# Kernel tuning notes

Hardware: AMD Instinct MI355X
Metric: run time of the kernel (lower is better)

The kernel has to match this reference:

```python
import jax, jax.numpy as jnp
import numpy as np

H = 64
VOCAB = 64
SLOTS = 8
EPS = 1e-5


def _layernorm(x, gamma, beta):
    mu = jnp.mean(x, axis=-1, keepdims=True)
    var = jnp.mean(jnp.square(x - mu), axis=-1, keepdims=True)
    return (x - mu) * jax.lax.rsqrt(var + EPS) * gamma + beta


def setup_inputs() -> dict:
    key = jax.random.key(0)
    ks = jax.random.split(key, 20)
    B, L = 1024, 2048
    s = 0.05
    inp = {
        "seq": jax.random.randint(ks[0], (B, L), 0, VOCAB, dtype=jnp.int64),
        "embed": jax.random.normal(ks[1], (VOCAB, H), jnp.float32) * s,
        "w1": jax.random.normal(ks[2], (2 * H, H), jnp.float32) * s,
        "b1": jnp.zeros((2 * H,), jnp.float32),
        "w2": jax.random.normal(ks[3], (H, 2 * H), jnp.float32) * s,
        "b2": jnp.zeros((H,), jnp.float32),
        "gamma": jnp.ones((H,), jnp.float32),
        "beta": jnp.zeros((H,), jnp.float32),
        "gate_w": jax.random.normal(ks[4], (1, H), jnp.float32) * s,
        "gate_b": jnp.zeros((1,), jnp.float32),
        "qi_w": jax.random.normal(ks[5], (H, H), jnp.float32) * s,
        "qi_b": jnp.zeros((H,), jnp.float32),
        "sk_w": jax.random.normal(ks[6], (H, H), jnp.float32) * s,
        "sk_b": jnp.zeros((H,), jnp.float32),
        "qr_w": jax.random.normal(ks[7], (H, H), jnp.float32) * s,
        "qr_b": jnp.zeros((H,), jnp.float32),
        "out_w": jax.random.normal(ks[8], (VOCAB, H), jnp.float32) * s,
        "out_b": jnp.zeros((VOCAB,), jnp.float32),
    }
    return inp


def reference(seq, embed, w1, b1, w2, b2, gamma, beta, gate_w, gate_b,
              qi_w, qi_b, sk_w, sk_b, qr_w, qr_b, out_w, out_b):
    # Encoder: embed -> FF residual -> LayerNorm
    h0 = embed[seq]                                  # [B, L, H]
    ff = jax.nn.relu(h0 @ w1.T + b1) @ w2.T + b2     # [B, L, H]
    h = _layernorm(h0 + ff, gamma, beta)             # [B, L, H]

    # Top-k gate over sequence -> gather memory slots
    scores = jnp.squeeze(h @ gate_w.T, -1) + gate_b[0]   # [B, L]
    _, idx = jax.lax.top_k(scores, SLOTS)                # [B, S]
    memory = jnp.take_along_axis(h, idx[:, :, None], axis=1)  # [B, S, H]

    scale = 1.0 / jnp.sqrt(jnp.float32(H))

    # Stage 1: initial read attention over slot keys
    q_init = h[:, -1, :] @ qi_w.T + qi_b                 # [B, H]
    slot_keys = memory @ sk_w.T + sk_b                   # [B, S, H]
    r_attn = jax.nn.softmax(jnp.einsum('bsh,bh->bs', slot_keys, q_init) * scale, axis=-1)
    read = jnp.einsum('bs,bsh->bh', r_attn, memory)
    q_refined = q_init + (read @ qr_w.T + qr_b)          # [B, H]

    # Stage 2: refined attention directly over memory
    attn = jax.nn.softmax(jnp.einsum('bsh,bh->bs', memory, q_refined) * scale, axis=-1)
    pooled = jnp.einsum('bs,bsh->bh', attn, memory)      # [B, H]
    return pooled @ out_w.T + out_b                      # [B, VOCAB]
```

## Files before the change

### kernel.cpp

```cpp
#include <hip/hip_runtime.h>
#include <hip/hip_bf16.h>

#define HD 64
#define LSEQ 2048
#define NBATCH 1024
#define NSLOTS 8

__global__ __launch_bounds__(128) void build_tables_kernel(
    const float* __restrict__ embed, const float* __restrict__ w1, const float* __restrict__ b1,
    const float* __restrict__ w2, const float* __restrict__ b2,
    const float* __restrict__ gamma, const float* __restrict__ beta,
    const float* __restrict__ gate_w, const float* __restrict__ gate_b,
    const float* __restrict__ qi_w, const float* __restrict__ qi_b,
    const float* __restrict__ sk_w, const float* __restrict__ sk_b,
    float* __restrict__ h_table, float* __restrict__ qi_table, float* __restrict__ sk_table,
    float* __restrict__ score)
{
    const int v = blockIdx.x;
    const int tid = threadIdx.x;

    __shared__ __align__(16) float E[HD];
    __shared__ __align__(16) float T1[2 * HD];
    __shared__ __align__(16) float Hrow[HD];

    if (tid < HD) E[tid] = embed[v * HD + tid];
    __syncthreads();

    {
        const float4* w1r = (const float4*)(w1 + tid * HD);
        const float4* E4  = (const float4*)E;
        float t = b1[tid];
        #pragma unroll
        for (int k = 0; k < HD / 4; ++k) {
            float4 a = w1r[k], e = E4[k];
            t = fmaf(a.x, e.x, t); t = fmaf(a.y, e.y, t);
            t = fmaf(a.z, e.z, t); t = fmaf(a.w, e.w, t);
        }
        T1[tid] = fmaxf(t, 0.0f);
    }
    __syncthreads();

    if (tid < HD) {
        const float4* w2r = (const float4*)(w2 + tid * 2 * HD);
        const float4* T4  = (const float4*)T1;
        float x = E[tid] + b2[tid];
        #pragma unroll
        for (int j = 0; j < 2 * HD / 4; ++j) {
            float4 a = w2r[j], t = T4[j];
            x = fmaf(a.x, t.x, x); x = fmaf(a.y, t.y, x);
            x = fmaf(a.z, t.z, x); x = fmaf(a.w, t.w, x);
        }
        float mu = x;
        #pragma unroll
        for (int off = 1; off < 64; off <<= 1) mu += __shfl_xor(mu, off);
        mu *= (1.0f / 64.0f);
        float d = x - mu;
        float var = d * d;
        #pragma unroll
        for (int off = 1; off < 64; off <<= 1) var += __shfl_xor(var, off);
        var *= (1.0f / 64.0f);
        float h = d * rsqrtf(var + 1e-5f) * gamma[tid] + beta[tid];
        Hrow[tid] = h;
        h_table[v * HD + tid] = h;

        float sc = h * gate_w[tid];
        #pragma unroll
        for (int off = 1; off < 64; off <<= 1) sc += __shfl_xor(sc, off);
        if (tid == 0) score[v] = sc + gate_b[0];
    }
    __syncthreads();

    {
        const int i = tid & 63;
        const float* W  = (tid < HD) ? qi_w : sk_w;
        const float* Bv = (tid < HD) ? qi_b : sk_b;
        const float4* Wr = (const float4*)(W + i * HD);
        const float4* H4 = (const float4*)Hrow;
        float acc = Bv[i];
        #pragma unroll
        for (int k = 0; k < HD / 4; ++k) {
            float4 a = Wr[k], h = H4[k];
            acc = fmaf(a.x, h.x, acc); acc = fmaf(a.y, h.y, acc);
            acc = fmaf(a.z, h.z, acc); acc = fmaf(a.w, h.w, acc);
        }
        float* dst = (tid < HD) ? qi_table : sk_table;
        dst[v * HD + i] = acc;
    }
}

__global__ __launch_bounds__(256) void main_kernel(
    const int* __restrict__ seq,
    const float* __restrict__ h_table, const float* __restrict__ qi_table,
    const float* __restrict__ sk_table,
    const float* __restrict__ qr_w, const float* __restrict__ qr_b,
    const float* __restrict__ out_w, const float* __restrict__ out_b,
    const float* __restrict__ score,
    float* __restrict__ out)
{
    const int b    = blockIdx.x;
    const int tid  = threadIdx.x;
    const int w    = tid >> 6;
    const int lane = tid & 63;

    __shared__ int   hist[4][65];
    __shared__ int   slot_tok[NSLOTS];
    __shared__ float sbuf[64];
    __shared__ int   order_s[64];
    __shared__ int   cntb[64];
    __shared__ int   last_s;
    __shared__ __align__(16) float rbuf[64];

    hist[w][lane] = 0;
    if (tid < 64) sbuf[tid] = score[tid];

    const int4* srow4 = (const int4*)(seq + (size_t)b * LSEQ);
    int4 a0 = srow4[tid];
    int4 a1 = srow4[256 + tid];
    if (tid == 255) last_s = a1.w;
    __syncthreads();

    atomicAdd(&hist[w][a0.x], 1); atomicAdd(&hist[w][a0.y], 1);
    atomicAdd(&hist[w][a0.z], 1); atomicAdd(&hist[w][a0.w], 1);
    atomicAdd(&hist[w][a1.x], 1); atomicAdd(&hist[w][a1.y], 1);
    atomicAdd(&hist[w][a1.z], 1); atomicAdd(&hist[w][a1.w], 1);
    __syncthreads();

    if (tid < 64) {
        int cnt = hist[0][tid] + hist[1][tid] + hist[2][tid] + hist[3][tid];
        float st = sbuf[tid];
        int rank = 0;
        for (int u = 0; u < 64; ++u) {
            float su = sbuf[u];
            if (su > st || (su == st && u < tid)) ++rank;
        }
        order_s[rank] = tid;
        hist[0][tid] = cnt;
    }
    __syncthreads();

    if (tid < 64) cntb[tid] = hist[0][order_s[tid]];
    __syncthreads();

    if (tid < 64) {
        int cum = 0;
        for (int u = 0; u < tid; ++u) cum += cntb[u];
        int cnt = cntb[tid];
        int tok = order_s[tid];
        #pragma unroll
        for (int s = 0; s < NSLOTS; ++s)
            if (s >= cum && s < cum + cnt) slot_tok[s] = tok;
    }
    __syncthreads();

    float qk = 0.0f;
    float mrow[NSLOTS];
    const float scale = 0.125f;

    if (tid < 64) {
        int st_[NSLOTS];
        #pragma unroll
        for (int s = 0; s < NSLOTS; ++s) st_[s] = slot_tok[s];

        qk = qi_table[last_s * HD + lane];

        float skrow[NSLOTS];
        #pragma unroll
        for (int s = 0; s < NSLOTS; ++s) {
            mrow[s]  = h_table[st_[s] * HD + lane];
            skrow[s] = sk_table[st_[s] * HD + lane];
        }

        float p[NSLOTS];
        #pragma unroll
        for (int s = 0; s < NSLOTS; ++s) p[s] = skrow[s] * qk;
        #pragma unroll
        for (int off = 1; off < 64; off <<= 1) {
            #pragma unroll
            for (int s = 0; s < NSLOTS; ++s) p[s] += __shfl_xor(p[s], off);
        }
        #pragma unroll
        for (int s = 0; s < NSLOTS; ++s) p[s] *= scale;
        float mx = p[0];
        #pragma unroll
        for (int s = 1; s < NSLOTS; ++s) mx = fmaxf(mx, p[s]);
        float sum = 0.0f, r[NSLOTS];
        #pragma unroll
        for (int s = 0; s < NSLOTS; ++s) { r[s] = expf(p[s] - mx); sum += r[s]; }
        float inv = 1.0f / sum;
        float readk = 0.0f;
        #pragma unroll
        for (int s = 0; s < NSLOTS; ++s) readk = fmaf(r[s] * inv, mrow[s], readk);
        rbuf[lane] = readk;
    }
    __syncthreads();

    float qref = 0.0f;
    if (tid < 64) {
        qref = qk + qr_b[lane];
        const float4* wr = (const float4*)(qr_w + lane * HD);
        const float4* r4 = (const float4*)rbuf;
        #pragma unroll
        for (int j = 0; j < HD / 4; ++j) {
            float4 a = wr[j], rv = r4[j];
            qref = fmaf(a.x, rv.x, qref); qref = fmaf(a.y, rv.y, qref);
            qref = fmaf(a.z, rv.z, qref); qref = fmaf(a.w, rv.w, qref);
        }

        float p2[NSLOTS];
        #pragma unroll
        for (int s = 0; s < NSLOTS; ++s) p2[s] = mrow[s] * qref;
        #pragma unroll
        for (int off = 1; off < 64; off <<= 1) {
            #pragma unroll
            for (int s = 0; s < NSLOTS; ++s) p2[s] += __shfl_xor(p2[s], off);
        }
        #pragma unroll
        for (int s = 0; s < NSLOTS; ++s) p2[s] *= scale;
        float mx = p2[0];
        #pragma unroll
        for (int s = 1; s < NSLOTS; ++s) mx = fmaxf(mx, p2[s]);
        float sum = 0.0f, a[NSLOTS];
        #pragma unroll
        for (int s = 0; s < NSLOTS; ++s) { a[s] = expf(p2[s] - mx); sum += a[s]; }
        float inv = 1.0f / sum;
        float pooled = 0.0f;
        #pragma unroll
        for (int s = 0; s < NSLOTS; ++s) pooled = fmaf(a[s] * inv, mrow[s], pooled);
        rbuf[lane] = pooled;
    }
    __syncthreads();

    if (tid < 64) {
        float acc = out_b[lane];
        const float4* wr = (const float4*)(out_w + lane * HD);
        const float4* r4 = (const float4*)rbuf;
        #pragma unroll
        for (int k = 0; k < HD / 4; ++k) {
            float4 a = wr[k], rv = r4[k];
            acc = fmaf(a.x, rv.x, acc); acc = fmaf(a.y, rv.y, acc);
            acc = fmaf(a.z, rv.z, acc); acc = fmaf(a.w, rv.w, acc);
        }
        out[(size_t)b * HD + lane] = acc;
    }
}

extern "C" void kernel_launch(void* const* d_in, const int* in_sizes, int n_in,
                              void* d_out, int out_size, void* d_ws, size_t ws_size,
                              hipStream_t stream) {
    const int*   seq    = (const int*)  d_in[0];
    const float* embed  = (const float*)d_in[1];
    const float* w1     = (const float*)d_in[2];
    const float* b1     = (const float*)d_in[3];
    const float* w2     = (const float*)d_in[4];
    const float* b2     = (const float*)d_in[5];
    const float* gamma  = (const float*)d_in[6];
    const float* beta   = (const float*)d_in[7];
    const float* gate_w = (const float*)d_in[8];
    const float* gate_b = (const float*)d_in[9];
    const float* qi_w   = (const float*)d_in[10];
    const float* qi_b   = (const float*)d_in[11];
    const float* sk_w   = (const float*)d_in[12];
    const float* sk_b   = (const float*)d_in[13];
    const float* qr_w   = (const float*)d_in[14];
    const float* qr_b   = (const float*)d_in[15];
    const float* out_w  = (const float*)d_in[16];
    const float* out_b  = (const float*)d_in[17];

    float* ws = (float*)d_ws;
    float* h_table  = ws;
    float* qi_table = ws + 4096;
    float* sk_table = ws + 8192;
    float* score    = ws + 12288;

    hipLaunchKernelGGL(build_tables_kernel, dim3(64), dim3(128), 0, stream,
                       embed, w1, b1, w2, b2, gamma, beta, gate_w, gate_b,
                       qi_w, qi_b, sk_w, sk_b,
                       h_table, qi_table, sk_table, score);

    hipLaunchKernelGGL(main_kernel, dim3(NBATCH), dim3(256), 0, stream,
                       seq, h_table, qi_table, sk_table,
                       qr_w, qr_b, out_w, out_b, score, (float*)d_out);
}
```

Baseline: 22.87 us.

## Fuse table build into main kernel with one wave per batch row

```diff
diff --git a/kernel.cpp b/kernel.cpp
--- a/kernel.cpp
+++ b/kernel.cpp
@@ -6,242 +6,268 @@
 #define NBATCH 1024
 #define NSLOTS 8
 
-__global__ __launch_bounds__(128) void build_tables_kernel(
+__global__ __launch_bounds__(512) void fused_kernel(
+    const int* __restrict__ seq,
     const float* __restrict__ embed, const float* __restrict__ w1, const float* __restrict__ b1,
     const float* __restrict__ w2, const float* __restrict__ b2,
     const float* __restrict__ gamma, const float* __restrict__ beta,
     const float* __restrict__ gate_w, const float* __restrict__ gate_b,
     const float* __restrict__ qi_w, const float* __restrict__ qi_b,
     const float* __restrict__ sk_w, const float* __restrict__ sk_b,
-    float* __restrict__ h_table, float* __restrict__ qi_table, float* __restrict__ sk_table,
-    float* __restrict__ score)
-{
-    const int v = blockIdx.x;
-    const int tid = threadIdx.x;
-
-    __shared__ __align__(16) float E[HD];
-    __shared__ __align__(16) float T1[2 * HD];
-    __shared__ __align__(16) float Hrow[HD];
-
-    if (tid < HD) E[tid] = embed[v * HD + tid];
-    __syncthreads();
-
-    {
-        const float4* w1r = (const float4*)(w1 + tid * HD);
-        const float4* E4  = (const float4*)E;
-        float t = b1[tid];
-        #pragma unroll
-        for (int k = 0; k < HD / 4; ++k) {
-            float4 a = w1r[k], e = E4[k];
-            t = fmaf(a.x, e.x, t); t = fmaf(a.y, e.y, t);
-            t = fmaf(a.z, e.z, t); t = fmaf(a.w, e.w, t);
-        }
-        T1[tid] = fmaxf(t, 0.0f);
-    }
-    __syncthreads();
-
-    if (tid < HD) {
-        const float4* w2r = (const float4*)(w2 + tid * 2 * HD);
-        const float4* T4  = (const float4*)T1;
-        float x = E[tid] + b2[tid];
-        #pragma unroll
-        for (int j = 0; j < 2 * HD / 4; ++j) {
-            float4 a = w2r[j], t = T4[j];
-            x = fmaf(a.x, t.x, x); x = fmaf(a.y, t.y, x);
-            x = fmaf(a.z, t.z, x); x = fmaf(a.w, t.w, x);
-        }
-        float mu = x;
-        #pragma unroll
-        for (int off = 1; off < 64; off <<= 1) mu += __shfl_xor(mu, off);
-        mu *= (1.0f / 64.0f);
-        float d = x - mu;
-        float var = d * d;
-        #pragma unroll
-        for (int off = 1; off < 64; off <<= 1) var += __shfl_xor(var, off);
-        var *= (1.0f / 64.0f);
-        float h = d * rsqrtf(var + 1e-5f) * gamma[tid] + beta[tid];
-        Hrow[tid] = h;
-        h_table[v * HD + tid] = h;
-
-        float sc = h * gate_w[tid];
-        #pragma unroll
-        for (int off = 1; off < 64; off <<= 1) sc += __shfl_xor(sc, off);
-        if (tid == 0) score[v] = sc + gate_b[0];
-    }
-    __syncthreads();
-
-    {
-        const int i = tid & 63;
-        const float* W  = (tid < HD) ? qi_w : sk_w;
-        const float* Bv = (tid < HD) ? qi_b : sk_b;
-        const float4* Wr = (const float4*)(W + i * HD);
-        const float4* H4 = (const float4*)Hrow;
-        float acc = Bv[i];
-        #pragma unroll
-        for (int k = 0; k < HD / 4; ++k) {
-            float4 a = Wr[k], h = H4[k];
-            acc = fmaf(a.x, h.x, acc); acc = fmaf(a.y, h.y, acc);
-            acc = fmaf(a.z, h.z, acc); acc = fmaf(a.w, h.w, acc);
-        }
-        float* dst = (tid < HD) ? qi_table : sk_table;
-        dst[v * HD + i] = acc;
-    }
-}
-
-__global__ __launch_bounds__(256) void main_kernel(
-    const int* __restrict__ seq,
-    const float* __restrict__ h_table, const float* __restrict__ qi_table,
-    const float* __restrict__ sk_table,
     const float* __restrict__ qr_w, const float* __restrict__ qr_b,
     const float* __restrict__ out_w, const float* __restrict__ out_b,
-    const float* __restrict__ score,
     float* __restrict__ out)
 {
-    const int b    = blockIdx.x;
     const int tid  = threadIdx.x;
     const int w    = tid >> 6;
     const int lane = tid & 63;
-
-    __shared__ int   hist[4][65];
-    __shared__ int   slot_tok[NSLOTS];
-    __shared__ float sbuf[64];
-    __shared__ int   order_s[64];
-    __shared__ int   cntb[64];
-    __shared__ int   last_s;
-    __shared__ __align__(16) float rbuf[64];
+    const int wu   = __builtin_amdgcn_readfirstlane(w);
+    const int row  = blockIdx.x * 8 + wu;
+
+    __shared__ float E [64][65];
+    __shared__ float T1[64][129];
+    __shared__ float X [64][65];
+    __shared__ float H [64][65];
+    __shared__ float QI[64][65];
+    __shared__ float SK[64][65];
+    __shared__ float score_s[64];
+    __shared__ int   hist[8][64];
+    __shared__ int   order_s[8][64];
+    __shared__ int   slot_s[8][NSLOTS];
+    __shared__ float rbuf[8][64];
+
+    const int4* srow4 = (const int4*)(seq + (size_t)row * LSEQ);
+    int4 q[8];
+    #pragma unroll
+    for (int i = 0; i < 8; ++i) q[i] = srow4[lane + 64 * i];
+
+    for (int i = tid; i < 64 * HD; i += 512) E[i >> 6][i & 63] = embed[i];
+    __syncthreads();
+
+    {
+        const int j0 = wu * 16;
+        float acc[16];
+        #pragma unroll
+        for (int jj = 0; jj < 16; ++jj) acc[jj] = b1[j0 + jj];
+        #pragma unroll 1
+        for (int half = 0; half < 2; ++half) {
+            float er[32];
+            #pragma unroll
+            for (int c = 0; c < 32; ++c) er[c] = E[lane][half * 32 + c];
+            #pragma unroll
+            for (int jj = 0; jj < 16; ++jj) {
+                const float* w1r = w1 + (j0 + jj) * HD + half * 32;
+                #pragma unroll
+                for (int c = 0; c < 32; ++c)
+                    acc[jj] = fmaf(er[c], w1r[c], acc[jj]);
+            }
+        }
+        #pragma unroll
+        for (int jj = 0; jj < 16; ++jj)
+            T1[lane][j0 + jj] = fmaxf(acc[jj], 0.0f);
+    }
+    __syncthreads();
+
+    {
+        const int i0 = wu * 8;
+        float acc[8];
+        #pragma unroll
+        for (int ii = 0; ii < 8; ++ii) acc[ii] = E[lane][i0 + ii] + b2[i0 + ii];
+        #pragma unroll 1
+        for (int quar = 0; quar < 4; ++quar) {
+            float tr[32];
+            #pragma unroll
+            for (int c = 0; c < 32; ++c) tr[c] = T1[lane][quar * 32 + c];
+            #pragma unroll
+            for (int ii = 0; ii < 8; ++ii) {
+                const float* w2r = w2 + (i0 + ii) * 2 * HD + quar * 32;
+                #pragma unroll
+                for (int c = 0; c < 32; ++c)
+                    acc[ii] = fmaf(tr[c], w2r[c], acc[ii]);
+            }
+        }
+        #pragma unroll
+        for (int ii = 0; ii < 8; ++ii) X[lane][i0 + ii] = acc[ii];
+    }
+    __syncthreads();
+
+    {
+        const int v  = tid >> 3;
+        const int g  = tid & 7;
+        const int k0 = g * 8;
+        float xr[8];
+        #pragma unroll
+        for (int d = 0; d < 8; ++d) xr[d] = X[v][k0 + d];
+        float s = 0.0f;
+        #pragma unroll
+        for (int d = 0; d < 8; ++d) s += xr[d];
+        s += __shfl_xor(s, 1); s += __shfl_xor(s, 2); s += __shfl_xor(s, 4);
+        const float mu = s * (1.0f / 64.0f);
+        float vs = 0.0f;
+        #pragma unroll
+        for (int d = 0; d < 8; ++d) { float dd = xr[d] - mu; vs = fmaf(dd, dd, vs); }
+        vs += __shfl_xor(vs, 1); vs += __shfl_xor(vs, 2); vs += __shfl_xor(vs, 4);
+        const float rstd = rsqrtf(vs * (1.0f / 64.0f) + 1e-5f);
+        float sp = 0.0f;
+        #pragma unroll
+        for (int d = 0; d < 8; ++d) {
+            const int k = k0 + d;
+            const float h = (xr[d] - mu) * rstd * gamma[k] + beta[k];
+            H[v][k] = h;
+            sp = fmaf(h, gate_w[k], sp);
+        }
+        sp += __shfl_xor(sp, 1); sp += __shfl_xor(sp, 2); sp += __shfl_xor(sp, 4);
+        if (g == 0) score_s[v] = sp + gate_b[0];
+    }
+    __syncthreads();
+
+    {
+        const bool isqi = (wu < 4);
+        const int  i0   = (wu & 3) * 16;
+        const float* Wm = isqi ? qi_w : sk_w;
+        const float* Bm = isqi ? qi_b : sk_b;
+        float acc[16];
+        #pragma unroll
+        for (int ii = 0; ii < 16; ++ii) acc[ii] = Bm[i0 + ii];
+        #pragma unroll 1
+        for (int half = 0; half < 2; ++half) {
+            float hr[32];
+            #pragma unroll
+            for (int c = 0; c < 32; ++c) hr[c] = H[lane][half * 32 + c];
+            #pragma unroll
+            for (int ii = 0; ii < 16; ++ii) {
+                const float* Wr = Wm + (i0 + ii) * HD + half * 32;
+                #pragma unroll
+                for (int c = 0; c < 32; ++c)
+                    acc[ii] = fmaf(hr[c], Wr[c], acc[ii]);
+            }
+        }
+        float (*DST)[65] = isqi ? QI : SK;
+        #pragma unroll
+        for (int ii = 0; ii < 16; ++ii) DST[lane][i0 + ii] = acc[ii];
+    }
+    __syncthreads();
 
     hist[w][lane] = 0;
-    if (tid < 64) sbuf[tid] = score[tid];
-
-    const int4* srow4 = (const int4*)(seq + (size_t)b * LSEQ);
-    int4 a0 = srow4[tid];
-    int4 a1 = srow4[256 + tid];
-    if (tid == 255) last_s = a1.w;
-    __syncthreads();
-
-    atomicAdd(&hist[w][a0.x], 1); atomicAdd(&hist[w][a0.y], 1);
-    atomicAdd(&hist[w][a0.z], 1); atomicAdd(&hist[w][a0.w], 1);
-    atomicAdd(&hist[w][a1.x], 1); atomicAdd(&hist[w][a1.y], 1);
-    atomicAdd(&hist[w][a1.z], 1); atomicAdd(&hist[w][a1.w], 1);
-    __syncthreads();
-
-    if (tid < 64) {
-        int cnt = hist[0][tid] + hist[1][tid] + hist[2][tid] + hist[3][tid];
-        float st = sbuf[tid];
-        int rank = 0;
-        for (int u = 0; u < 64; ++u) {
-            float su = sbuf[u];
-            if (su > st || (su == st && u < tid)) ++rank;
-        }
-        order_s[rank] = tid;
-        hist[0][tid] = cnt;
-    }
-    __syncthreads();
-
-    if (tid < 64) cntb[tid] = hist[0][order_s[tid]];
-    __syncthreads();
-
-    if (tid < 64) {
-        int cum = 0;
-        for (int u = 0; u < tid; ++u) cum += cntb[u];
-        int cnt = cntb[tid];
-        int tok = order_s[tid];
-        #pragma unroll
-        for (int s = 0; s < NSLOTS; ++s)
-            if (s >= cum && s < cum + cnt) slot_tok[s] = tok;
-    }
-    __syncthreads();
-
-    float qk = 0.0f;
-    float mrow[NSLOTS];
+    #pragma unroll
+    for (int i = 0; i < 8; ++i) {
+        atomicAdd(&hist[w][q[i].x], 1); atomicAdd(&hist[w][q[i].y], 1);
+        atomicAdd(&hist[w][q[i].z], 1); atomicAdd(&hist[w][q[i].w], 1);
+    }
+    const int last = __shfl(q[7].w, 63);
+
+    const float sc = score_s[lane];
+    int rank = 0;
+    #pragma unroll
+    for (int u = 0; u < 64; ++u) {
+        float su = __shfl(sc, u);
+        if (su > sc || (su == sc && u < lane)) ++rank;
+    }
+    order_s[w][rank] = lane;
+    __syncthreads();
+
+    const int tok  = order_s[w][lane];
+    const int cntr = hist[w][tok];
+
+    int inc = cntr;
+    #pragma unroll
+    for (int off = 1; off < 64; off <<= 1) {
+        int v2 = __shfl_up(inc, off);
+        if (lane >= off) inc += v2;
+    }
+    const int cum = inc - cntr;
+    #pragma unroll
+    for (int s = 0; s < NSLOTS; ++s)
+        if (s >= cum && s < cum + cntr) slot_s[w][s] = tok;
+    __syncthreads();
+
+    int st_[NSLOTS];
+    #pragma unroll
+    for (int s = 0; s < NSLOTS; ++s) st_[s] = slot_s[w][s];
+
     const float scale = 0.125f;
-
-    if (tid < 64) {
-        int st_[NSLOTS];
-        #pragma unroll
-        for (int s = 0; s < NSLOTS; ++s) st_[s] = slot_tok[s];
-
-        qk = qi_table[last_s * HD + lane];
-
-        float skrow[NSLOTS];
-        #pragma unroll
-        for (int s = 0; s < NSLOTS; ++s) {
-            mrow[s]  = h_table[st_[s] * HD + lane];
-            skrow[s] = sk_table[st_[s] * HD + lane];
-        }
-
-        float p[NSLOTS];
-        #pragma unroll
-        for (int s = 0; s < NSLOTS; ++s) p[s] = skrow[s] * qk;
-        #pragma unroll
-        for (int off = 1; off < 64; off <<= 1) {
-            #pragma unroll
-            for (int s = 0; s < NSLOTS; ++s) p[s] += __shfl_xor(p[s], off);
-        }
-        #pragma unroll
-        for (int s = 0; s < NSLOTS; ++s) p[s] *= scale;
-        float mx = p[0];
-        #pragma unroll
-        for (int s = 1; s < NSLOTS; ++s) mx = fmaxf(mx, p[s]);
-        float sum = 0.0f, r[NSLOTS];
-        #pragma unroll
-        for (int s = 0; s < NSLOTS; ++s) { r[s] = expf(p[s] - mx); sum += r[s]; }
-        float inv = 1.0f / sum;
-        float readk = 0.0f;
-        #pragma unroll
-        for (int s = 0; s < NSLOTS; ++s) readk = fmaf(r[s] * inv, mrow[s], readk);
-        rbuf[lane] = readk;
-    }
-    __syncthreads();
-
-    float qref = 0.0f;
-    if (tid < 64) {
-        qref = qk + qr_b[lane];
+    const float qk = QI[last][lane];
+
+    float mrow[NSLOTS], skrow[NSLOTS];
+    #pragma unroll
+    for (int s = 0; s < NSLOTS; ++s) {
+        mrow[s]  = H[st_[s]][lane];
+        skrow[s] = SK[st_[s]][lane];
+    }
+
+    float p[NSLOTS];
+    #pragma unroll
+    for (int s = 0; s < NSLOTS; ++s) p[s] = skrow[s] * qk;
+    #pragma unroll
+    for (int off = 1; off < 64; off <<= 1) {
+        #pragma unroll
+        for (int s = 0; s < NSLOTS; ++s) p[s] += __shfl_xor(p[s], off);
+    }
+    #pragma unroll
+    for (int s = 0; s < NSLOTS; ++s) p[s] *= scale;
+    float mx = p[0];
+    #pragma unroll
+    for (int s = 1; s < NSLOTS; ++s) mx = fmaxf(mx, p[s]);
+    float sum = 0.0f, r[NSLOTS];
+    #pragma unroll
+    for (int s = 0; s < NSLOTS; ++s) { r[s] = expf(p[s] - mx); sum += r[s]; }
+    float inv = 1.0f / sum;
+    float readk = 0.0f;
+    #pragma unroll
+    for (int s = 0; s < NSLOTS; ++s) readk = fmaf(r[s] * inv, mrow[s], readk);
+    rbuf[w][lane] = readk;
+    __syncthreads();
+
+    float qref = qk + qr_b[lane];
+    {
         const float4* wr = (const float4*)(qr_w + lane * HD);
-        const float4* r4 = (const float4*)rbuf;
-        #pragma unroll
-        for (int j = 0; j < HD / 4; ++j) {
-            float4 a = wr[j], rv = r4[j];
-            qref = fmaf(a.x, rv.x, qref); qref = fmaf(a.y, rv.y, qref);
-            qref = fmaf(a.z, rv.z, qref); qref = fmaf(a.w, rv.w, qref);
-        }
-
-        float p2[NSLOTS];
-        #pragma unroll
-        for (int s = 0; s < NSLOTS; ++s) p2[s] = mrow[s] * qref;
-        #pragma unroll
-        for (int off = 1; off < 64; off <<= 1) {
-            #pragma unroll
-            for (int s = 0; s < NSLOTS; ++s) p2[s] += __shfl_xor(p2[s], off);
-        }
-        #pragma unroll
-        for (int s = 0; s < NSLOTS; ++s) p2[s] *= scale;
-        float mx = p2[0];
-        #pragma unroll
-        for (int s = 1; s < NSLOTS; ++s) mx = fmaxf(mx, p2[s]);
-        float sum = 0.0f, a[NSLOTS];
-        #pragma unroll
-        for (int s = 0; s < NSLOTS; ++s) { a[s] = expf(p2[s] - mx); sum += a[s]; }
-        float inv = 1.0f / sum;
-        float pooled = 0.0f;
-        #pragma unroll
-        for (int s = 0; s < NSLOTS; ++s) pooled = fmaf(a[s] * inv, mrow[s], pooled);
-        rbuf[lane] = pooled;
-    }
-    __syncthreads();
-
-    if (tid < 64) {
-        float acc = out_b[lane];
-        const float4* wr = (const float4*)(out_w + lane * HD);
-        const float4* r4 = (const float4*)rbuf;
-        #pragma unroll
-        for (int k = 0; k < HD / 4; ++k) {
-            float4 a = wr[k], rv = r4[k];
-            acc = fmaf(a.x, rv.x, acc); acc = fmaf(a.y, rv.y, acc);
-            acc = fmaf(a.z, rv.z, acc); acc = fmaf(a.w, rv.w, acc);
-        }
-        out[(size_t)b * HD + lane] = acc;
-    }
+        #pragma unroll
+        for (int j4 = 0; j4 < HD / 4; ++j4) {
+            float4 a = wr[j4];
+            qref = fmaf(a.x, rbuf[w][4 * j4 + 0], qref);
+            qref = fmaf(a.y, rbuf[w][4 * j4 + 1], qref);
+            qref = fmaf(a.z, rbuf[w][4 * j4 + 2], qref);
+            qref = fmaf(a.w, rbuf[w][4 * j4 + 3], qref);
+        }
+    }
+
+    float p2[NSLOTS];
+    #pragma unroll
+    for (int s = 0; s < NSLOTS; ++s) p2[s] = mrow[s] * qref;
+    #pragma unroll
+    for (int off = 1; off < 64; off <<= 1) {
+        #pragma unroll
+        for (int s = 0; s < NSLOTS; ++s) p2[s] += __shfl_xor(p2[s], off);
+    }
+    #pragma unroll
+    for (int s = 0; s < NSLOTS; ++s) p2[s] *= scale;
+    float mx2 = p2[0];
+    #pragma unroll
+    for (int s = 1; s < NSLOTS; ++s) mx2 = fmaxf(mx2, p2[s]);
+    float sum2 = 0.0f, aa[NSLOTS];
+    #pragma unroll
+    for (int s = 0; s < NSLOTS; ++s) { aa[s] = expf(p2[s] - mx2); sum2 += aa[s]; }
+    float inv2 = 1.0f / sum2;
+    float pooled = 0.0f;
+    #pragma unroll
+    for (int s = 0; s < NSLOTS; ++s) pooled = fmaf(aa[s] * inv2, mrow[s], pooled);
+    __syncthreads();
+    rbuf[w][lane] = pooled;
+    __syncthreads();
+
+    float acc = out_b[lane];
+    {
+        const float4* wo = (const float4*)(out_w + lane * HD);
+        #pragma unroll
+        for (int k4 = 0; k4 < HD / 4; ++k4) {
+            float4 a = wo[k4];
+            acc = fmaf(a.x, rbuf[w][4 * k4 + 0], acc);
+            acc = fmaf(a.y, rbuf[w][4 * k4 + 1], acc);
+            acc = fmaf(a.z, rbuf[w][4 * k4 + 2], acc);
+            acc = fmaf(a.w, rbuf[w][4 * k4 + 3], acc);
+        }
+    }
+    out[(size_t)row * HD + lane] = acc;
 }
 
 extern "C" void kernel_launch(void* const* d_in, const int* in_sizes, int n_in,
@@ -266,18 +292,8 @@
     const float* out_w  = (const float*)d_in[16];
     const float* out_b  = (const float*)d_in[17];
 
-    float* ws = (float*)d_ws;
-    float* h_table  = ws;
-    float* qi_table = ws + 4096;
-    float* sk_table = ws + 8192;
-    float* score    = ws + 12288;
-
-    hipLaunchKernelGGL(build_tables_kernel, dim3(64), dim3(128), 0, stream,
-                       embed, w1, b1, w2, b2, gamma, beta, gate_w, gate_b,
-                       qi_w, qi_b, sk_w, sk_b,
-                       h_table, qi_table, sk_table, score);
-
-    hipLaunchKernelGGL(main_kernel, dim3(NBATCH), dim3(256), 0, stream,
-                       seq, h_table, qi_table, sk_table,
-                       qr_w, qr_b, out_w, out_b, score, (float*)d_out);
+    hipLaunchKernelGGL(fused_kernel, dim3(NBATCH / 8), dim3(512), 0, stream,
+                       seq, embed, w1, b1, w2, b2, gamma, beta, gate_w, gate_b,
+                       qi_w, qi_b, sk_w, sk_b, qr_w, qr_b, out_w, out_b,
+                       (float*)d_out);
 }
```

Measured after the change: 58.34 us. +155.1%, slower.

## Process one batch row per wavefront instead of one row per block

Applied to the files above, without the earlier changes.

```diff
diff --git a/kernel.cpp b/kernel.cpp
--- a/kernel.cpp
+++ b/kernel.cpp
@@ -25,7 +25,6 @@
 
     if (tid < HD) E[tid] = embed[v * HD + tid];
     __syncthreads();
-
     {
         const float4* w1r = (const float4*)(w1 + tid * HD);
         const float4* E4  = (const float4*)E;
@@ -39,7 +38,6 @@
         T1[tid] = fmaxf(t, 0.0f);
     }
     __syncthreads();
-
     if (tid < HD) {
         const float4* w2r = (const float4*)(w2 + tid * 2 * HD);
         const float4* T4  = (const float4*)T1;
@@ -62,14 +60,12 @@
         float h = d * rsqrtf(var + 1e-5f) * gamma[tid] + beta[tid];
         Hrow[tid] = h;
         h_table[v * HD + tid] = h;
-
         float sc = h * gate_w[tid];
         #pragma unroll
         for (int off = 1; off < 64; off <<= 1) sc += __shfl_xor(sc, off);
         if (tid == 0) score[v] = sc + gate_b[0];
     }
     __syncthreads();
-
     {
         const int i = tid & 63;
         const float* W  = (tid < HD) ? qi_w : sk_w;
@@ -97,151 +93,142 @@
     const float* __restrict__ score,
     float* __restrict__ out)
 {
-    const int b    = blockIdx.x;
     const int tid  = threadIdx.x;
     const int w    = tid >> 6;
     const int lane = tid & 63;
-
-    __shared__ int   hist[4][65];
-    __shared__ int   slot_tok[NSLOTS];
-    __shared__ float sbuf[64];
-    __shared__ int   order_s[64];
-    __shared__ int   cntb[64];
-    __shared__ int   last_s;
-    __shared__ __align__(16) float rbuf[64];
+    const int row  = blockIdx.x * 4 + w;
+
+    __shared__ int   hist[4][64];
+    __shared__ int   order_s[4][64];
+    __shared__ int   slot_s[4][NSLOTS];
+    __shared__ float rbuf[4][64];
+
+    const int4* srow4 = (const int4*)(seq + (size_t)row * LSEQ);
+    int4 q[8];
+    #pragma unroll
+    for (int i = 0; i < 8; ++i) q[i] = srow4[lane + 64 * i];
+
+    const float sc = score[lane];
 
     hist[w][lane] = 0;
-    if (tid < 64) sbuf[tid] = score[tid];
-
-    const int4* srow4 = (const int4*)(seq + (size_t)b * LSEQ);
-    int4 a0 = srow4[tid];
-    int4 a1 = srow4[256 + tid];
-    if (tid == 255) last_s = a1.w;
-    __syncthreads();
-
-    atomicAdd(&hist[w][a0.x], 1); atomicAdd(&hist[w][a0.y], 1);
-    atomicAdd(&hist[w][a0.z], 1); atomicAdd(&hist[w][a0.w], 1);
-    atomicAdd(&hist[w][a1.x], 1); atomicAdd(&hist[w][a1.y], 1);
-    atomicAdd(&hist[w][a1.z], 1); atomicAdd(&hist[w][a1.w], 1);
-    __syncthreads();
-
-    if (tid < 64) {
-        int cnt = hist[0][tid] + hist[1][tid] + hist[2][tid] + hist[3][tid];
-        float st = sbuf[tid];
-        int rank = 0;
-        for (int u = 0; u < 64; ++u) {
-            float su = sbuf[u];
-            if (su > st || (su == st && u < tid)) ++rank;
-        }
-        order_s[rank] = tid;
-        hist[0][tid] = cnt;
-    }
-    __syncthreads();
-
-    if (tid < 64) cntb[tid] = hist[0][order_s[tid]];
-    __syncthreads();
-
-    if (tid < 64) {
-        int cum = 0;
-        for (int u = 0; u < tid; ++u) cum += cntb[u];
-        int cnt = cntb[tid];
-        int tok = order_s[tid];
-        #pragma unroll
-        for (int s = 0; s < NSLOTS; ++s)
-            if (s >= cum && s < cum + cnt) slot_tok[s] = tok;
-    }
-    __syncthreads();
-
-    float qk = 0.0f;
-    float mrow[NSLOTS];
+    #pragma unroll
+    for (int i = 0; i < 8; ++i) {
+        atomicAdd(&hist[w][q[i].x], 1); atomicAdd(&hist[w][q[i].y], 1);
+        atomicAdd(&hist[w][q[i].z], 1); atomicAdd(&hist[w][q[i].w], 1);
+    }
+    const int last = __shfl(q[7].w, 63);
+
+    int rank = 0;
+    #pragma unroll
+    for (int u = 0; u < 64; ++u) {
+        float su = __shfl(sc, u);
+        if (su > sc || (su == sc && u < lane)) ++rank;
+    }
+    order_s[w][rank] = lane;
+    __syncthreads();
+
+    const int tok  = order_s[w][lane];
+    const int cntr = hist[w][tok];
+
+    int inc = cntr;
+    #pragma unroll
+    for (int off = 1; off < 64; off <<= 1) {
+        int v2 = __shfl_up(inc, off);
+        if (lane >= off) inc += v2;
+    }
+    const int cum = inc - cntr;
+    #pragma unroll
+    for (int s = 0; s < NSLOTS; ++s)
+        if (s >= cum && s < cum + cntr) slot_s[w][s] = tok;
+    __syncthreads();
+
+    int st_[NSLOTS];
+    #pragma unroll
+    for (int s = 0; s < NSLOTS; ++s) st_[s] = slot_s[w][s];
+
     const float scale = 0.125f;
-
-    if (tid < 64) {
-        int st_[NSLOTS];
-        #pragma unroll
-        for (int s = 0; s < NSLOTS; ++s) st_[s] = slot_tok[s];
-
-        qk = qi_table[last_s * HD + lane];
-
-        float skrow[NSLOTS];
-        #pragma unroll
-        for (int s = 0; s < NSLOTS; ++s) {
-            mrow[s]  = h_table[st_[s] * HD + lane];
-            skrow[s] = sk_table[st_[s] * HD + lane];
-        }
-
-        float p[NSLOTS];
-        #pragma unroll
-        for (int s = 0; s < NSLOTS; ++s) p[s] = skrow[s] * qk;
-        #pragma unroll
-        for (int off = 1; off < 64; off <<= 1) {
-            #pragma unroll
-            for (int s = 0; s < NSLOTS; ++s) p[s] += __shfl_xor(p[s], off);
-        }
-        #pragma unroll
-        for (int s = 0; s < NSLOTS; ++s) p[s] *= scale;
-        float mx = p[0];
-        #pragma unroll
-        for (int s = 1; s < NSLOTS; ++s) mx = fmaxf(mx, p[s]);
-        float sum = 0.0f, r[NSLOTS];
-        #pragma unroll
-        for (int s = 0; s < NSLOTS; ++s) { r[s] = expf(p[s] - mx); sum += r[s]; }
-        float inv = 1.0f / sum;
-        float readk = 0.0f;
-        #pragma unroll
-        for (int s = 0; s < NSLOTS; ++s) readk = fmaf(r[s] * inv, mrow[s], readk);
-        rbuf[lane] = readk;
-    }
-    __syncthreads();
-
-    float qref = 0.0f;
-    if (tid < 64) {
-        qref = qk + qr_b[lane];
+    const float qk = qi_table[last * HD + lane];
+
+    float mrow[NSLOTS], skrow[NSLOTS];
+    #pragma unroll
+    for (int s = 0; s < NSLOTS; ++s) {
+        mrow[s]  = h_table[st_[s] * HD + lane];
+        skrow[s] = sk_table[st_[s] * HD + lane];
+    }
+
+    float p[NSLOTS];
+    #pragma unroll
+    for (int s = 0; s < NSLOTS; ++s) p[s] = skrow[s] * qk;
+    #pragma unroll
+    for (int off = 1; off < 64; off <<= 1) {
+        #pragma unroll
+        for (int s = 0; s < NSLOTS; ++s) p[s] += __shfl_xor(p[s], off);
+    }
+    #pragma unroll
+    for (int s = 0; s < NSLOTS; ++s) p[s] *= scale;
+    float mx = p[0];
+    #pragma unroll
+    for (int s = 1; s < NSLOTS; ++s) mx = fmaxf(mx, p[s]);
+    float sum = 0.0f, r[NSLOTS];
+    #pragma unroll
+    for (int s = 0; s < NSLOTS; ++s) { r[s] = expf(p[s] - mx); sum += r[s]; }
+    float inv = 1.0f / sum;
+    float readk = 0.0f;
+    #pragma unroll
+    for (int s = 0; s < NSLOTS; ++s) readk = fmaf(r[s] * inv, mrow[s], readk);
+    rbuf[w][lane] = readk;
+    __syncthreads();
+
+    float qref = qk + qr_b[lane];
+    {
         const float4* wr = (const float4*)(qr_w + lane * HD);
-        const float4* r4 = (const float4*)rbuf;
-        #pragma unroll
-        for (int j = 0; j < HD / 4; ++j) {
-            float4 a = wr[j], rv = r4[j];
-            qref = fmaf(a.x, rv.x, qref); qref = fmaf(a.y, rv.y, qref);
-            qref = fmaf(a.z, rv.z, qref); qref = fmaf(a.w, rv.w, qref);
-        }
-
-        float p2[NSLOTS];
-        #pragma unroll
-        for (int s = 0; s < NSLOTS; ++s) p2[s] = mrow[s] * qref;
-        #pragma unroll
-        for (int off = 1; off < 64; off <<= 1) {
-            #pragma unroll
-            for (int s = 0; s < NSLOTS; ++s) p2[s] += __shfl_xor(p2[s], off);
-        }
-        #pragma unroll
-        for (int s = 0; s < NSLOTS; ++s) p2[s] *= scale;
-        float mx = p2[0];
-        #pragma unroll
-        for (int s = 1; s < NSLOTS; ++s) mx = fmaxf(mx, p2[s]);
-        float sum = 0.0f, a[NSLOTS];
-        #pragma unroll
-        for (int s = 0; s < NSLOTS; ++s) { a[s] = expf(p2[s] - mx); sum += a[s]; }
-        float inv = 1.0f / sum;
-        float pooled = 0.0f;
-        #pragma unroll
-        for (int s = 0; s < NSLOTS; ++s) pooled = fmaf(a[s] * inv, mrow[s], pooled);
-        rbuf[lane] = pooled;
-    }
-    __syncthreads();
-
-    if (tid < 64) {
-        float acc = out_b[lane];
-        const float4* wr = (const float4*)(out_w + lane * HD);
-        const float4* r4 = (const float4*)rbuf;
-        #pragma unroll
-        for (int k = 0; k < HD / 4; ++k) {
-            float4 a = wr[k], rv = r4[k];
-            acc = fmaf(a.x, rv.x, acc); acc = fmaf(a.y, rv.y, acc);
-            acc = fmaf(a.z, rv.z, acc); acc = fmaf(a.w, rv.w, acc);
-        }
-        out[(size_t)b * HD + lane] = acc;
-    }
+        #pragma unroll
+        for (int j4 = 0; j4 < HD / 4; ++j4) {
+            float4 a = wr[j4];
+            qref = fmaf(a.x, rbuf[w][4 * j4 + 0], qref);
+            qref = fmaf(a.y, rbuf[w][4 * j4 + 1], qref);
+            qref = fmaf(a.z, rbuf[w][4 * j4 + 2], qref);
+            qref = fmaf(a.w, rbuf[w][4 * j4 + 3], qref);
+        }
+    }
+
+    float p2[NSLOTS];
+    #pragma unroll
+    for (int s = 0; s < NSLOTS; ++s) p2[s] = mrow[s] * qref;
+    #pragma unroll
+    for (int off = 1; off < 64; off <<= 1) {
+        #pragma unroll
+        for (int s = 0; s < NSLOTS; ++s) p2[s] += __shfl_xor(p2[s], off);
+    }
+    #pragma unroll
+    for (int s = 0; s < NSLOTS; ++s) p2[s] *= scale;
+    float mx2 = p2[0];
+    #pragma unroll
+    for (int s = 1; s < NSLOTS; ++s) mx2 = fmaxf(mx2, p2[s]);
+    float sum2 = 0.0f, aa[NSLOTS];
+    #pragma unroll
+    for (int s = 0; s < NSLOTS; ++s) { aa[s] = expf(p2[s] - mx2); sum2 += aa[s]; }
+    float inv2 = 1.0f / sum2;
+    float pooled = 0.0f;
+    #pragma unroll
+    for (int s = 0; s < NSLOTS; ++s) pooled = fmaf(aa[s] * inv2, mrow[s], pooled);
+    __syncthreads();
+    rbuf[w][lane] = pooled;
+    __syncthreads();
+
+    float acc = out_b[lane];
+    {
+        const float4* wo = (const float4*)(out_w + lane * HD);
+        #pragma unroll
+        for (int k4 = 0; k4 < HD / 4; ++k4) {
+            float4 a = wo[k4];
+            acc = fmaf(a.x, rbuf[w][4 * k4 + 0], acc);
+            acc = fmaf(a.y, rbuf[w][4 * k4 + 1], acc);
+            acc = fmaf(a.z, rbuf[w][4 * k4 + 2], acc);
+            acc = fmaf(a.w, rbuf[w][4 * k4 + 3], acc);
+        }
+    }
+    out[(size_t)row * HD + lane] = acc;
 }
 
 extern "C" void kernel_launch(void* const* d_in, const int* in_sizes, int n_in,
@@ -277,7 +264,7 @@
                        qi_w, qi_b, sk_w, sk_b,
                        h_table, qi_table, sk_table, score);
 
-    hipLaunchKernelGGL(main_kernel, dim3(NBATCH), dim3(256), 0, stream,
+    hipLaunchKernelGGL(main_kernel, dim3(NBATCH / 4), dim3(256), 0, stream,
                        seq, h_table, qi_table, sk_table,
                        qr_w, qr_b, out_w, out_b, score, (float*)d_out);
 }
```

Result: no change. 23.14 us (+1.2%).
